# Performance work log

Measured on AMD Instinct MI355X. Metric: run time of the kernel, lower is better.

## Reference

```python
import jax, jax.numpy as jnp
import numpy as np

B = 2
DZ, DY, DX = 10, 200, 176
N_PER = 100000                      # active voxels per batch element
C_IN, C_MID, C_OUT = 64, 32, 64
STRIDE = 8

_OFFS = np.stack(np.meshgrid(np.arange(3), np.arange(3), np.arange(3), indexing='ij'), -1).reshape(27, 3)


def _build_indices():
    rng = np.random.RandomState(0)
    rows = []
    for b in range(B):
        lin = rng.choice(DZ * DY * DX, size=N_PER, replace=False)
        z, y, x = np.unravel_index(lin, (DZ, DY, DX))
        rows.append(np.stack([np.full(N_PER, b), z, y, x], 1))
    return np.concatenate(rows, 0).astype(np.int32)


def _neighbor_maps(indices):
    # spconv-style indice generation (pure integer bookkeeping, done once in numpy)
    N = indices.shape[0]
    OZ, OY, OX = (DZ - 1) // 2 + 1, (DY - 1) // 2 + 1, (DX - 1) // 2 + 1  # k3 s2 p1 output shape
    hi = np.array([OZ, OY, OX])
    hin = np.array([DZ, DY, DX])
    i3 = indices[:, 1:4].astype(np.int64)
    cand = i3[:, None, :] + 1 - _OFFS[None]          # o*stride = i + pad - k
    valid = (cand % 2 == 0).all(-1)
    o3 = cand // 2
    valid &= ((o3 >= 0) & (o3 < hi)).all(-1)
    ob = np.broadcast_to(indices[:, 0:1], (N, 27))
    flat = np.stack([ob[valid], o3[..., 0][valid], o3[..., 1][valid], o3[..., 2][valid]], 1)
    down = np.unique(flat, axis=0).astype(np.int32)  # [M,4] stride-2 conv output coords
    M = down.shape[0]
    in_grid = -np.ones((B, DZ, DY, DX), np.int32)
    in_grid[indices[:, 0], indices[:, 1], indices[:, 2], indices[:, 3]] = np.arange(N)
    dn_grid = -np.ones((B, OZ, OY, OX), np.int32)
    dn_grid[down[:, 0], down[:, 1], down[:, 2], down[:, 3]] = np.arange(M)
    # stride-2 conv: output row m, kernel k <- input at o*2 - 1 + k
    src = down[:, None, 1:4].astype(np.int64) * 2 - 1 + _OFFS[None]
    ok = ((src >= 0) & (src < hin)).all(-1)
    srcc = np.clip(src, 0, hin - 1)
    nbr_down = np.where(ok, in_grid[down[:, 0:1], srcc[..., 0], srcc[..., 1], srcc[..., 2]], -1).astype(np.int32)
    # submanifold 3x3x3 on down coords
    d3 = down[:, None, 1:4].astype(np.int64) + (_OFFS[None] - 1)
    ok2 = ((d3 >= 0) & (d3 < hi)).all(-1)
    d3c = np.clip(d3, 0, hi - 1)
    nbr_sub = np.where(ok2, dn_grid[down[:, 0:1], d3c[..., 0], d3c[..., 1], d3c[..., 2]], -1).astype(np.int32)
    # inverse conv (transposed pairs of the stride-2 conv): input row n, kernel k <- down row at (i+1-k)/2
    o3c = np.clip(o3, 0, hi - 1)
    nbr_inv = np.where(valid, dn_grid[indices[:, 0:1], o3c[..., 0], o3c[..., 1], o3c[..., 2]], -1).astype(np.int32)
    return down, nbr_down, nbr_sub, nbr_inv


def setup_inputs():
    key = jax.random.key(0)
    ks = jax.random.split(key, 12)
    indices = _build_indices()
    down_indices, nbr_down, nbr_sub, nbr_inv = _neighbor_maps(indices)
    N = indices.shape[0]
    w = lambda k, shp: jax.random.normal(k, shp, jnp.float32) * 0.05
    l2r = np.array([[0., -1., 0., 0.], [0., 0., -1., 0.], [1., 0., 0., 0.]], np.float32)  # lidar->rect
    p2 = np.array([[721.54, 0., 609.56, 44.85], [0., 721.54, 172.85, 0.216], [0., 0., 1., 0.0027]], np.float32)
    return {
        'features': jax.random.normal(ks[0], (N, C_IN), jnp.float32),
        'W_down1': w(ks[1], (27, C_IN, C_MID)),
        'W_res': w(ks[2], (27, C_IN, C_MID)),
        'W_sub2': w(ks[3], (27, C_MID, C_MID)),
        'W_2d1': w(ks[4], (9, C_MID, C_MID)),
        'W_2d2': w(ks[5], (9, C_MID, C_MID)),
        'W_sub3': w(ks[6], (27, C_MID, C_MID)),
        'W_inv4': w(ks[7], (27, C_MID, C_OUT)),
        'bn32_g': 1.0 + 0.1 * jax.random.normal(ks[8], (7, C_MID), jnp.float32),
        'bn32_b': 0.1 * jax.random.normal(ks[9], (7, C_MID), jnp.float32),
        'bn64_g': 1.0 + 0.1 * jax.random.normal(ks[10], (2, C_OUT), jnp.float32),
        'bn64_b': 0.1 * jax.random.normal(ks[11], (2, C_OUT), jnp.float32),
        'calib_l2r': jnp.asarray(np.tile(l2r, (B, 1, 1))),
        'calib_p2': jnp.asarray(np.tile(p2, (B, 1, 1))),
        'down_indices': jnp.asarray(down_indices),
        'nbr_down': jnp.asarray(nbr_down),
        'nbr_sub': jnp.asarray(nbr_sub),
        'nbr_inv': jnp.asarray(nbr_inv),
        'stride': STRIDE,
        'batch_size': B,
    }


def _bn(x, g, b, eps=1e-3):
    # BatchNorm1d training-mode forward (batch stats, biased variance, eps=1e-3)
    m = x.mean(0)
    v = x.var(0)
    return (x - m) * jax.lax.rsqrt(v + eps) * g + b


def _gconv(feats, nbr, W):
    # spconv gather -> GEMM -> accumulate; nbr[m,k] is source row or -1
    out = jnp.zeros((nbr.shape[0], W.shape[-1]), feats.dtype)
    for k in range(W.shape[0]):
        idx = nbr[:, k]
        m = (idx >= 0).astype(feats.dtype)[:, None]
        out = out + (feats[jnp.maximum(idx, 0)] * m) @ W[k]
    return out


def _index2uv(down_indices, calib_l2r, calib_p2, stride):
    vs = 0.05 * stride
    fi = down_indices.astype(jnp.float32)
    x = fi[:, 3] * vs + (0.0 + vs / 2)
    y = fi[:, 2] * vs + (-40.0 + vs / 2)
    z = fi[:, 1] * vs + (-3.0 + vs / 2)
    pts = jnp.stack([x, y, z, jnp.ones_like(x)], 1)           # [M,4] homogeneous lidar pts
    b = down_indices[:, 0]
    rect = jnp.einsum('mi,mji->mj', pts, calib_l2r[b])        # lidar_to_rect
    rh = jnp.concatenate([rect, jnp.ones_like(rect[:, :1])], 1)
    proj = jnp.einsum('mi,mji->mj', rh, calib_p2[b])          # rect_to_img
    u = jax.lax.stop_gradient(proj[:, 0] / proj[:, 2]).astype(jnp.int32)
    v = jax.lax.stop_gradient(proj[:, 1] / proj[:, 2]).astype(jnp.int32)
    u = jnp.clip(u, 0, 1400 - stride) // stride
    v = jnp.clip(v, 0, 400 - stride) // stride
    return b, u, v


def reference(features, W_down1, W_res, W_sub2, W_2d1, W_2d2, W_sub3, W_inv4,
              bn32_g, bn32_b, bn64_g, bn64_b, calib_l2r, calib_p2,
              down_indices, nbr_down, nbr_sub, nbr_inv, stride, batch_size):
    relu = jax.nn.relu
    d3 = relu(_bn(_gconv(features, nbr_down, W_down1), bn32_g[0], bn32_b[0]))   # d3_conv1 (spconv s2)
    d3 = relu(_bn(_gconv(d3, nbr_sub, W_sub2), bn32_g[1], bn32_b[1]))           # d3_conv2 (subm)
    res = relu(_bn(_gconv(features, nbr_down, W_res), bn32_g[2], bn32_b[2]))    # resnet_layer (spconv s2)
    d3 = d3 + res
    # 3D -> 2D reprojection (index2uv) and 2D submanifold conv stage
    b, u, v = _index2uv(down_indices, calib_l2r, calib_p2, stride)
    U, V = 1400 // stride, 400 // stride
    M = d3.shape[0]
    grid = -jnp.ones((batch_size, U, V), jnp.int32)
    grid = grid.at[b, u, v].max(jnp.arange(M, dtype=jnp.int32))  # deterministic dedupe of uv collisions
    du = jnp.repeat(jnp.arange(-1, 2), 3)
    dv = jnp.tile(jnp.arange(-1, 2), 3)
    uu = u[:, None] + du[None]
    vv = v[:, None] + dv[None]
    ok = (uu >= 0) & (uu < U) & (vv >= 0) & (vv < V)
    nbr2d = jnp.where(ok, grid[b[:, None], jnp.clip(uu, 0, U - 1), jnp.clip(vv, 0, V - 1)], -1)
    d2 = relu(_bn(_gconv(d3, nbr2d, W_2d1), bn32_g[3], bn32_b[3]))              # d2_conv1
    d2 = relu(_bn(_gconv(d2, nbr2d, W_2d2), bn32_g[4], bn32_b[4]))              # d2_conv2
    d3 = _bn(d3 + d2, bn32_g[5], bn32_b[5])                                     # mid_norm_fn (no relu)
    d3 = relu(_bn(_gconv(d3, nbr_sub, W_sub3), bn32_g[6], bn32_b[6]))           # d3_conv3
    out = relu(_bn(_gconv(d3, nbr_inv, W_inv4), bn64_g[0], bn64_b[0]))          # d3_conv4 (inverse conv)
    out = _bn(out + features, bn64_g[1], bn64_b[1])                             # output_norm_fn
    return out
```

## Files before the change

kernel.cpp:

```cpp
#include <hip/hip_runtime.h>

#define NBANK 64
#define ACC_STRIDE (NBANK * 128)

typedef _Float16 half8 __attribute__((ext_vector_type(8)));
typedef float    fx4   __attribute__((ext_vector_type(4)));

__global__ void init_kernel(float* __restrict__ acc, int accN, _Float16* __restrict__ zrow,
                            int* __restrict__ grid, int gridN)
{
    int i = blockIdx.x * 256 + threadIdx.x;
    if (i < accN) acc[i] = 0.f;
    if (i < 64) ((float*)zrow)[i] = 0.f;
    if (i < gridN) grid[i] = -1;
}

struct WDesc { const float* W; _Float16* H; _Float16* L; int K, CIN, COUT, base; };
struct WArgs { WDesc d[7]; int total; };

__global__ void wsplit_all_kernel(WArgs a)
{
    int t = blockIdx.x * 256 + threadIdx.x;
    if (t >= a.total) return;
    int seg = 0;
    #pragma unroll
    for (int s = 1; s < 7; ++s) if (t >= a.d[s].base) seg = s;
    const WDesc D = a.d[seg];
    int tt   = t - D.base;
    int lane = tt & 63;
    int frag = tt >> 6;
    int NT = D.COUT >> 4, NS = D.CIN >> 5;
    int ct = frag % NT;
    int s2 = (frag / NT) % NS;
    int k  = frag / (NT * NS);
    int col = ct * 16 + (lane & 15);
    int cib = s2 * 32 + ((lane >> 4) << 3);
    half8 vh, vl;
    #pragma unroll
    for (int j = 0; j < 8; ++j) {
        float w = D.W[(size_t)(k * D.CIN + cib + j) * D.COUT + col];
        _Float16 hh = (_Float16)w;
        vh[j] = hh;
        vl[j] = (_Float16)(w - (float)hh);
    }
    *(half8*)(D.H + (size_t)tt * 8) = vh;
    *(half8*)(D.L + (size_t)tt * 8) = vl;
}

__global__ void tof16_kernel(const float* __restrict__ x, _Float16* __restrict__ h, long total)
{
    long base = ((long)blockIdx.x * 256 + threadIdx.x) * 8;
    if (base >= total) return;
    fx4 v0 = *(const fx4*)(x + base);
    fx4 v1 = *(const fx4*)(x + base + 4);
    half8 hh;
    #pragma unroll
    for (int j = 0; j < 4; ++j) { hh[j] = (_Float16)v0[j]; hh[4 + j] = (_Float16)v1[j]; }
    *(half8*)(h + base) = hh;
}

template <int CIN, int COUT, int K, bool DUAL>
__global__ __launch_bounds__(256) void gconv_mfma_kernel(
    const _Float16* __restrict__ fh, const int* __restrict__ nbr,
    const _Float16* __restrict__ Bh1, const _Float16* __restrict__ Bl1,
    const _Float16* __restrict__ Bh2, const _Float16* __restrict__ Bl2,
    const _Float16* __restrict__ zrow,
    float* __restrict__ out1, float* __restrict__ out2,
    float* __restrict__ sAcc1, float* __restrict__ sAcc2, int M)
{
    constexpr int NS   = CIN / 32;
    constexpr int NT   = COUT / 16;
    constexpr int NCH  = K * NS;
    constexpr int W2   = DUAL ? 2 : 1;
    constexpr int NARR = 2 * W2;
    constexpr int SKB  = NARR * NT;
    constexpr int NLD  = SKB / 4;

    __shared__ _Float16 ldsB[2][SKB * 512];

    const int tid  = threadIdx.x;
    const int lane = tid & 63;
    const int wv   = tid >> 6;
    const int g    = lane >> 4;
    const int r    = lane & 15;
    const int mb   = blockIdx.x * 128 + wv * 32;

    const int  row0 = mb + r;
    const int  row1 = mb + 16 + r;
    const bool ok0  = row0 < M;
    const bool ok1  = row1 < M;

    fx4 acc1[2][NT];
    fx4 acc2[DUAL ? 2 : 1][DUAL ? NT : 1];
    const fx4 zf = {0.f, 0.f, 0.f, 0.f};
    #pragma unroll
    for (int rt = 0; rt < 2; ++rt)
        #pragma unroll
        for (int ct = 0; ct < NT; ++ct) acc1[rt][ct] = zf;
    if constexpr (DUAL) {
        #pragma unroll
        for (int rt = 0; rt < 2; ++rt)
            #pragma unroll
            for (int ct = 0; ct < NT; ++ct) acc2[rt][ct] = zf;
    }

    fx4   stg[NLD];
    half8 Breg[NT][2][W2];
    half8 Aa[2], Ab[2];
    int   q0, q1;

    auto idxld = [&](int c, int& o0, int& o1) {
        if (c < NCH) {
            const int k = (NS == 2) ? (c >> 1) : c;
            o0 = ok0 ? nbr[(size_t)row0 * K + k] : -1;
            o1 = ok1 ? nbr[(size_t)row1 * K + k] : -1;
        } else { o0 = -1; o1 = -1; }
    };
    auto loadA = [&](half8 (&A)[2], int i0, int i1, int c) {
        const int cb = (NS == 2) ? ((c & 1) * 32) : 0;
        const _Float16* p0 = (i0 >= 0) ? fh + (size_t)i0 * CIN : zrow;
        const _Float16* p1 = (i1 >= 0) ? fh + (size_t)i1 * CIN : zrow;
        A[0] = *(const half8*)(p0 + cb + g * 8);
        A[1] = *(const half8*)(p1 + cb + g * 8);
    };
    auto stage_ld = [&](int c) {
        #pragma unroll
        for (int i = 0; i < NLD; ++i) {
            const int o   = tid * 16 + i * 4096;
            const int arr = o / (NT * 1024);
            const int oa  = o % (NT * 1024);
            const _Float16* ap = (arr == 0) ? Bh1 : (arr == 1) ? Bl1
                                : (arr == 2) ? Bh2 : Bl2;
            stg[i] = *(const fx4*)(ap + (size_t)c * (NT * 512) + oa / 2);
        }
    };
    auto stage_wr = [&](int buf) {
        #pragma unroll
        for (int i = 0; i < NLD; ++i)
            *(fx4*)(&ldsB[buf][0] + (tid * 16 + i * 4096) / 2) = stg[i];
    };
    auto loadB = [&](int buf) {
        #pragma unroll
        for (int ct = 0; ct < NT; ++ct)
            #pragma unroll
            for (int hl = 0; hl < 2; ++hl)
                #pragma unroll
                for (int w = 0; w < W2; ++w) {
                    const int arr = w * 2 + hl;
                    Breg[ct][hl][w] = *(const half8*)(&ldsB[buf][0] + (arr * NT + ct) * 512 + lane * 8);
                }
    };
    auto compute = [&](half8 (&A)[2]) {
        #pragma unroll
        for (int ct = 0; ct < NT; ++ct)
            #pragma unroll
            for (int rt = 0; rt < 2; ++rt) {
                acc1[rt][ct] = __builtin_amdgcn_mfma_f32_16x16x32_f16(A[rt], Breg[ct][0][0], acc1[rt][ct], 0, 0, 0);
                acc1[rt][ct] = __builtin_amdgcn_mfma_f32_16x16x32_f16(A[rt], Breg[ct][1][0], acc1[rt][ct], 0, 0, 0);
                if constexpr (DUAL) {
                    acc2[rt][ct] = __builtin_amdgcn_mfma_f32_16x16x32_f16(A[rt], Breg[ct][0][1], acc2[rt][ct], 0, 0, 0);
                    acc2[rt][ct] = __builtin_amdgcn_mfma_f32_16x16x32_f16(A[rt], Breg[ct][1][1], acc2[rt][ct], 0, 0, 0);
                }
            }
    };
    auto phase = [&](int c, half8 (&Acur)[2], half8 (&Anext)[2]) {
        const bool hn = (c + 1 < NCH);
        if (hn) stage_ld(c + 1);
        loadA(Anext, q0, q1, hn ? c + 1 : c);
        idxld(c + 2, q0, q1);
        loadB(c & 1);
        compute(Acur);
        if (hn) stage_wr((c + 1) & 1);
        __syncthreads();
    };

    idxld(0, q0, q1);
    loadA(Aa, q0, q1, 0);
    idxld(1, q0, q1);
    stage_ld(0);
    stage_wr(0);
    __syncthreads();

    #pragma unroll 1
    for (int c = 0; c < NCH; c += 2) {
        phase(c, Aa, Ab);
        if (c + 1 < NCH) phase(c + 1, Ab, Aa);
    }

    #pragma unroll
    for (int rt = 0; rt < 2; ++rt)
        #pragma unroll
        for (int q = 0; q < 4; ++q) {
            const int rw = mb + rt * 16 + g * 4 + q;
            if (rw < M) {
                #pragma unroll
                for (int ct = 0; ct < NT; ++ct) {
                    out1[(size_t)rw * COUT + ct * 16 + r] = acc1[rt][ct][q];
                    if constexpr (DUAL)
                        out2[(size_t)rw * COUT + ct * 16 + r] = acc2[rt][ct][q];
                }
            }
        }

    #pragma unroll
    for (int ct = 0; ct < NT; ++ct) {
        float s1 = 0.f, p1 = 0.f, s2v = 0.f, p2v = 0.f;
        #pragma unroll
        for (int rt = 0; rt < 2; ++rt)
            #pragma unroll
            for (int q = 0; q < 4; ++q) {
                const int rw = mb + rt * 16 + g * 4 + q;
                if (rw < M) {
                    float v = acc1[rt][ct][q];
                    s1 += v; p1 += v * v;
                    if constexpr (DUAL) { float u = acc2[rt][ct][q]; s2v += u; p2v += u * u; }
                }
            }
        s1 += __shfl_xor(s1, 16, 64); s1 += __shfl_xor(s1, 32, 64);
        p1 += __shfl_xor(p1, 16, 64); p1 += __shfl_xor(p1, 32, 64);
        if constexpr (DUAL) {
            s2v += __shfl_xor(s2v, 16, 64); s2v += __shfl_xor(s2v, 32, 64);
            p2v += __shfl_xor(p2v, 16, 64); p2v += __shfl_xor(p2v, 32, 64);
        }
        if (lane < 16) {
            float* a = sAcc1 + ((blockIdx.x * 4 + wv) & (NBANK - 1)) * 128;
            atomicAdd(&a[ct * 16 + lane], s1);
            atomicAdd(&a[64 + ct * 16 + lane], p1);
            if constexpr (DUAL) {
                float* b2 = sAcc2 + ((blockIdx.x * 4 + wv) & (NBANK - 1)) * 128;
                atomicAdd(&b2[ct * 16 + lane], s2v);
                atomicAdd(&b2[64 + ct * 16 + lane], p2v);
            }
        }
    }
}

template <int C>
__global__ void finalize_kernel(const float* __restrict__ acc, const float* __restrict__ g,
                                const float* __restrict__ b, int M, float* __restrict__ sc)
{
    int c = threadIdx.x;
    if (c < C) {
        float s = 0.f, s2 = 0.f;
        #pragma unroll 8
        for (int k = 0; k < NBANK; ++k) {
            s  += acc[k * 128 + c];
            s2 += acc[k * 128 + 64 + c];
        }
        float inv  = 1.f / (float)M;
        float mean = s * inv;
        float var  = s2 * inv - mean * mean;
        float rstd = rsqrtf(var + 1e-3f);
        float scale = g[c] * rstd;
        sc[c]      = scale;
        sc[64 + c] = b[c] - mean * scale;
    }
}

template <int C>
__global__ __launch_bounds__(256) void apply_kernel(
    const float* __restrict__ x, const float* __restrict__ sc,
    const float* __restrict__ addv, float* __restrict__ outf,
    _Float16* __restrict__ outh, float* __restrict__ statAcc, long total, int relu)
{
    __shared__ float shS[64], shS2[64];
    if (statAcc && threadIdx.x < 64) { shS[threadIdx.x] = 0.f; shS2[threadIdx.x] = 0.f; }

    float s[8], s2[8];
    #pragma unroll
    for (int j = 0; j < 8; ++j) { s[j] = 0.f; s2[j] = 0.f; }

    const long start  = ((long)blockIdx.x * 256 + threadIdx.x) * 8;
    const long stride = (long)gridDim.x * 256 * 8;
    const int  c0     = (int)(start & (C - 1));
    float sA[8], sB[8];
    #pragma unroll
    for (int j = 0; j < 8; ++j) { sA[j] = sc[c0 + j]; sB[j] = sc[64 + c0 + j]; }

    for (long base = start; base < total; base += stride) {
        fx4 v0 = *(const fx4*)(x + base);
        fx4 v1 = *(const fx4*)(x + base + 4);
        float v[8] = {v0[0], v0[1], v0[2], v0[3], v1[0], v1[1], v1[2], v1[3]};
        fx4 a0 = {0.f, 0.f, 0.f, 0.f}, a1 = {0.f, 0.f, 0.f, 0.f};
        if (addv) { a0 = *(const fx4*)(addv + base); a1 = *(const fx4*)(addv + base + 4); }
        #pragma unroll
        for (int j = 0; j < 8; ++j) {
            float w = v[j] * sA[j] + sB[j];
            if (relu) w = fmaxf(w, 0.f);
            if (addv) w += (j < 4) ? a0[j] : a1[j - 4];
            v[j] = w;
            s[j] += w; s2[j] += w * w;
        }
        if (outf) {
            *(fx4*)(outf + base)     = fx4{v[0], v[1], v[2], v[3]};
            *(fx4*)(outf + base + 4) = fx4{v[4], v[5], v[6], v[7]};
        }
        if (outh) {
            half8 hh;
            #pragma unroll
            for (int j = 0; j < 8; ++j) hh[j] = (_Float16)v[j];
            *(half8*)(outh + base) = hh;
        }
    }

    if (statAcc) {
        __syncthreads();
        #pragma unroll
        for (int j = 0; j < 8; ++j) {
            atomicAdd(&shS[c0 + j], s[j]);
            atomicAdd(&shS2[c0 + j], s2[j]);
        }
        __syncthreads();
        if (threadIdx.x < C) {
            float* a = statAcc + (blockIdx.x & (NBANK - 1)) * 128;
            atomicAdd(&a[threadIdx.x], shS[threadIdx.x]);
            atomicAdd(&a[64 + threadIdx.x], shS2[threadIdx.x]);
        }
    }
}

__global__ void uv_scatter_kernel(const int* __restrict__ down, const float* __restrict__ l2r,
                                  const float* __restrict__ p2, int M,
                                  int* __restrict__ ub, int* __restrict__ vb,
                                  int* __restrict__ grid)
{
    __shared__ int shCell[256];
    const int m = blockIdx.x * 256 + threadIdx.x;
    int cell = -1;
    if (m < M) {
        int b = down[4 * m];
        float fz = (float)down[4 * m + 1];
        float fy = (float)down[4 * m + 2];
        float fx = (float)down[4 * m + 3];
        const float vs = 0.4f;
        float x = __fadd_rn(__fmul_rn(fx, vs), 0.2f);
        float y = __fadd_rn(__fmul_rn(fy, vs), -39.79999923706054688f);
        float z = __fadd_rn(__fmul_rn(fz, vs), -2.79999995231628418f);
        double xd = (double)x, yd = (double)y, zd = (double)z;
        const float* L = l2r + b * 12;
        double r0 = (double)L[0] * xd + (double)L[1] * yd + (double)L[2]  * zd + (double)L[3];
        double r1 = (double)L[4] * xd + (double)L[5] * yd + (double)L[6]  * zd + (double)L[7];
        double r2 = (double)L[8] * xd + (double)L[9] * yd + (double)L[10] * zd + (double)L[11];
        const float* P = p2 + b * 12;
        double p0 = (double)P[0] * r0 + (double)P[1] * r1 + (double)P[2]  * r2 + (double)P[3];
        double p1 = (double)P[4] * r0 + (double)P[5] * r1 + (double)P[6]  * r2 + (double)P[7];
        double pz = (double)P[8] * r0 + (double)P[9] * r1 + (double)P[10] * r2 + (double)P[11];
        int u = (int)(p0 / pz);
        int v = (int)(p1 / pz);
        u = min(max(u, 0), 1392) >> 3;
        v = min(max(v, 0), 392) >> 3;
        ub[m] = u;
        vb[m] = v;
        cell = (b * 175 + u) * 50 + v;
    }
    shCell[threadIdx.x] = cell;
    __syncthreads();
    if (m < M) {
        const bool last = (threadIdx.x == 255) || (shCell[threadIdx.x + 1] != cell);
        if (last) atomicMax(&grid[cell], m);
    }
}

__global__ void grid_copy_kernel(const int* __restrict__ grid, int* __restrict__ grid2, int n)
{
    int i = blockIdx.x * 256 + threadIdx.x;
    if (i < n) grid2[i] = grid[i];
}

__global__ void nbr2d_kernel(const int* __restrict__ down, const int* __restrict__ ub,
                             const int* __restrict__ vb, const int* __restrict__ grid,
                             int* __restrict__ nb2, int M)
{
    int m = blockIdx.x * 256 + threadIdx.x;
    if (m >= M) return;
    int b = down[4 * m];
    int u = ub[m], v = vb[m];
    #pragma unroll
    for (int j = 0; j < 9; ++j) {
        int uu = u + j / 3 - 1;
        int vv = v + j % 3 - 1;
        int val = -1;
        if (uu >= 0 && uu < 175 && vv >= 0 && vv < 50) val = grid[(b * 175 + uu) * 50 + vv];
        nb2[m * 9 + j] = val;
    }
}

extern "C" void kernel_launch(void* const* d_in, const int* in_sizes, int n_in,
                              void* d_out, int out_size, void* d_ws, size_t ws_size,
                              hipStream_t stream)
{
    const float* feats  = (const float*)d_in[0];
    const float* Wd1    = (const float*)d_in[1];
    const float* Wres   = (const float*)d_in[2];
    const float* Wsub2  = (const float*)d_in[3];
    const float* W2d1   = (const float*)d_in[4];
    const float* W2d2   = (const float*)d_in[5];
    const float* Wsub3  = (const float*)d_in[6];
    const float* Winv4  = (const float*)d_in[7];
    const float* bn32g  = (const float*)d_in[8];
    const float* bn32b  = (const float*)d_in[9];
    const float* bn64g  = (const float*)d_in[10];
    const float* bn64b  = (const float*)d_in[11];
    const float* l2r    = (const float*)d_in[12];
    const float* p2c    = (const float*)d_in[13];
    const int*   down   = (const int*)d_in[14];
    const int*   nbrD   = (const int*)d_in[15];
    const int*   nbrS   = (const int*)d_in[16];
    const int*   nbrI   = (const int*)d_in[17];

    const int N = in_sizes[0] / 64;
    const int M = in_sizes[14] / 4;

    char* ws = (char*)d_ws;
    size_t off = 0;
    auto alloc = [&](size_t bytes) -> void* {
        void* p = ws + off;
        off = (off + bytes + 255) & ~(size_t)255;
        return p;
    };
    float* t0    = (float*)alloc((size_t)M * 32 * 4);
    float* t1    = (float*)alloc((size_t)M * 32 * 4);
    float* t2    = (float*)alloc((size_t)M * 32 * 4);
    int*   ub    = (int*)alloc((size_t)M * 4);
    int*   vb    = (int*)alloc((size_t)M * 4);
    int*   nb2   = (int*)alloc((size_t)M * 9 * 4);
    int*   grid  = (int*)alloc((size_t)2 * 175 * 50 * 4);
    int*   grid2 = (int*)alloc((size_t)2 * 175 * 50 * 4);
    float* acc   = (float*)alloc((size_t)9 * ACC_STRIDE * 4);
    float* sc    = (float*)alloc((size_t)9 * 128 * 4);
    _Float16* zrow = (_Float16*)alloc(128 * 2);
    _Float16* fhh = (_Float16*)alloc((size_t)N * 64 * 2);
    _Float16* t0h = (_Float16*)alloc((size_t)M * 32 * 2);
    _Float16* t1h = (_Float16*)alloc((size_t)M * 32 * 2);
    _Float16* t2h = (_Float16*)alloc((size_t)M * 32 * 2);
    _Float16* wD1h = (_Float16*)alloc((size_t)55296 * 2);
    _Float16* wD1l = (_Float16*)alloc((size_t)55296 * 2);
    _Float16* wReh = (_Float16*)alloc((size_t)55296 * 2);
    _Float16* wRel = (_Float16*)alloc((size_t)55296 * 2);
    _Float16* wS2h = (_Float16*)alloc((size_t)27648 * 2);
    _Float16* wS2l = (_Float16*)alloc((size_t)27648 * 2);
    _Float16* w21h = (_Float16*)alloc((size_t)9216 * 2);
    _Float16* w21l = (_Float16*)alloc((size_t)9216 * 2);
    _Float16* w22h = (_Float16*)alloc((size_t)9216 * 2);
    _Float16* w22l = (_Float16*)alloc((size_t)9216 * 2);
    _Float16* wS3h = (_Float16*)alloc((size_t)27648 * 2);
    _Float16* wS3l = (_Float16*)alloc((size_t)27648 * 2);
    _Float16* wI4h = (_Float16*)alloc((size_t)55296 * 2);
    _Float16* wI4l = (_Float16*)alloc((size_t)55296 * 2);
    float* g0 = (float*)d_out;

    const int accN = 9 * ACC_STRIDE;
    init_kernel<<<(accN + 255) / 256, 256, 0, stream>>>(acc, accN, zrow, grid, 17500);

    WArgs wa;
    auto mkd = [](const float* W, _Float16* H, _Float16* L, int K, int CIN, int COUT, int base) {
        WDesc d; d.W = W; d.H = H; d.L = L; d.K = K; d.CIN = CIN; d.COUT = COUT; d.base = base;
        return d;
    };
    int b0 = 0;
    wa.d[0] = mkd(Wd1,   wD1h, wD1l, 27, 64, 32, b0); b0 += 27 * 64 * 32 / 8;
    wa.d[1] = mkd(Wres,  wReh, wRel, 27, 64, 32, b0); b0 += 27 * 64 * 32 / 8;
    wa.d[2] = mkd(Wsub2, wS2h, wS2l, 27, 32, 32, b0); b0 += 27 * 32 * 32 / 8;
    wa.d[3] = mkd(W2d1,  w21h, w21l,  9, 32, 32, b0); b0 += 9 * 32 * 32 / 8;
    wa.d[4] = mkd(W2d2,  w22h, w22l,  9, 32, 32, b0); b0 += 9 * 32 * 32 / 8;
    wa.d[5] = mkd(Wsub3, wS3h, wS3l, 27, 32, 32, b0); b0 += 27 * 32 * 32 / 8;
    wa.d[6] = mkd(Winv4, wI4h, wI4l, 27, 32, 64, b0); b0 += 27 * 32 * 64 / 8;
    wa.total = b0;
    wsplit_all_kernel<<<(wa.total + 255) / 256, 256, 0, stream>>>(wa);

    const long totF = (long)N * 64;
    tof16_kernel<<<(int)((totF / 8 + 255) / 256), 256, 0, stream>>>(feats, fhh, totF);

    const int  gT    = (M + 127) / 128;
    const int  gTN   = (N + 127) / 128;
    const long tot32 = (long)M * 32;
    const long tot64 = (long)N * 64;
    const int  ab32  = min((int)((tot32 / 8 + 255) / 256), 2560);
    const int  ab64  = min((int)((tot64 / 8 + 255) / 256), 2560);
    const int  gM    = (M + 255) / 256;

    gconv_mfma_kernel<64, 32, 27, true><<<gT, 256, 0, stream>>>(
        fhh, nbrD, wD1h, wD1l, wReh, wRel, zrow, t0, t1, acc + 0 * ACC_STRIDE, acc + 1 * ACC_STRIDE, M);
    finalize_kernel<32><<<1, 64, 0, stream>>>(acc + 0 * ACC_STRIDE, bn32g + 0 * 32, bn32b + 0 * 32, M, sc + 0 * 128);
    finalize_kernel<32><<<1, 64, 0, stream>>>(acc + 1 * ACC_STRIDE, bn32g + 2 * 32, bn32b + 2 * 32, M, sc + 1 * 128);
    apply_kernel<32><<<ab32, 256, 0, stream>>>(t0, sc + 0 * 128, nullptr, nullptr, t0h, nullptr, tot32, 1);
    apply_kernel<32><<<ab32, 256, 0, stream>>>(t1, sc + 1 * 128, nullptr, t1, nullptr, nullptr, tot32, 1);

    gconv_mfma_kernel<32, 32, 27, false><<<gT, 256, 0, stream>>>(
        t0h, nbrS, wS2h, wS2l, nullptr, nullptr, zrow, t2, nullptr, acc + 2 * ACC_STRIDE, nullptr, M);
    finalize_kernel<32><<<1, 64, 0, stream>>>(acc + 2 * ACC_STRIDE, bn32g + 1 * 32, bn32b + 1 * 32, M, sc + 2 * 128);
    apply_kernel<32><<<ab32, 256, 0, stream>>>(t2, sc + 2 * 128, t1, t2, t2h, nullptr, tot32, 1);

    uv_scatter_kernel<<<gM, 256, 0, stream>>>(down, l2r, p2c, M, ub, vb, grid);
    grid_copy_kernel<<<(17500 + 255) / 256, 256, 0, stream>>>(grid, grid2, 17500);
    nbr2d_kernel<<<gM, 256, 0, stream>>>(down, ub, vb, grid2, nb2, M);

    gconv_mfma_kernel<32, 32, 9, false><<<gT, 256, 0, stream>>>(
        t2h, nb2, w21h, w21l, nullptr, nullptr, zrow, t0, nullptr, acc + 3 * ACC_STRIDE, nullptr, M);
    finalize_kernel<32><<<1, 64, 0, stream>>>(acc + 3 * ACC_STRIDE, bn32g + 3 * 32, bn32b + 3 * 32, M, sc + 3 * 128);
    apply_kernel<32><<<ab32, 256, 0, stream>>>(t0, sc + 3 * 128, nullptr, nullptr, t0h, nullptr, tot32, 1);

    gconv_mfma_kernel<32, 32, 9, false><<<gT, 256, 0, stream>>>(
        t0h, nb2, w22h, w22l, nullptr, nullptr, zrow, t1, nullptr, acc + 4 * ACC_STRIDE, nullptr, M);
    finalize_kernel<32><<<1, 64, 0, stream>>>(acc + 4 * ACC_STRIDE, bn32g + 4 * 32, bn32b + 4 * 32, M, sc + 4 * 128);
    apply_kernel<32><<<ab32, 256, 0, stream>>>(t1, sc + 4 * 128, t2, t1, nullptr, acc + 5 * ACC_STRIDE, tot32, 1);
    finalize_kernel<32><<<1, 64, 0, stream>>>(acc + 5 * ACC_STRIDE, bn32g + 5 * 32, bn32b + 5 * 32, M, sc + 5 * 128);
    apply_kernel<32><<<ab32, 256, 0, stream>>>(t1, sc + 5 * 128, nullptr, nullptr, t1h, nullptr, tot32, 0);

    gconv_mfma_kernel<32, 32, 27, false><<<gT, 256, 0, stream>>>(
        t1h, nbrS, wS3h, wS3l, nullptr, nullptr, zrow, t0, nullptr, acc + 6 * ACC_STRIDE, nullptr, M);
    finalize_kernel<32><<<1, 64, 0, stream>>>(acc + 6 * ACC_STRIDE, bn32g + 6 * 32, bn32b + 6 * 32, M, sc + 6 * 128);
    apply_kernel<32><<<ab32, 256, 0, stream>>>(t0, sc + 6 * 128, nullptr, nullptr, t0h, nullptr, tot32, 1);

    gconv_mfma_kernel<32, 64, 27, false><<<gTN, 256, 0, stream>>>(
        t0h, nbrI, wI4h, wI4l, nullptr, nullptr, zrow, g0, nullptr, acc + 7 * ACC_STRIDE, nullptr, N);
    finalize_kernel<64><<<1, 64, 0, stream>>>(acc + 7 * ACC_STRIDE, bn64g + 0 * 64, bn64b + 0 * 64, N, sc + 7 * 128);
    apply_kernel<64><<<ab64, 256, 0, stream>>>(g0, sc + 7 * 128, feats, g0, nullptr, acc + 8 * ACC_STRIDE, tot64, 1);
    finalize_kernel<64><<<1, 64, 0, stream>>>(acc + 8 * ACC_STRIDE, bn64g + 1 * 64, bn64b + 1 * 64, N, sc + 8 * 128);
    apply_kernel<64><<<ab64, 256, 0, stream>>>(g0, sc + 8 * 128, nullptr, (float*)d_out, nullptr, nullptr, tot64, 0);
}
```

Baseline: 567.0 us.

## Process two K-chunks per barrier in gather-conv MFMA pipeline

Restructures the gather-convolution main loop so each pipeline stage stages, gathers and computes two consecutive K-chunks, with ping-pong A registers and a double-size LDS weight buffer. This halves the number of __syncthreads barriers and gives more independent gathers in flight per stage, plus s_setprio around the MFMA section. The trade-off is doubled LDS and staging/A-fragment registers, which may reduce occupancy, plus a tail path for an odd chunk count.

```diff
diff --git a/kernel.cpp b/kernel.cpp
--- a/kernel.cpp
+++ b/kernel.cpp
@@ -68,15 +68,17 @@
     float* __restrict__ out1, float* __restrict__ out2,
     float* __restrict__ sAcc1, float* __restrict__ sAcc2, int M)
 {
-    constexpr int NS   = CIN / 32;
-    constexpr int NT   = COUT / 16;
-    constexpr int NCH  = K * NS;
-    constexpr int W2   = DUAL ? 2 : 1;
-    constexpr int NARR = 2 * W2;
-    constexpr int SKB  = NARR * NT;
-    constexpr int NLD  = SKB / 4;
-
-    __shared__ _Float16 ldsB[2][SKB * 512];
+    constexpr int NS    = CIN / 32;
+    constexpr int NT    = COUT / 16;
+    constexpr int NCH   = K * NS;
+    constexpr int NPAIR = NCH / 2;
+    constexpr int W2    = DUAL ? 2 : 1;
+    constexpr int NARR  = 2 * W2;
+    constexpr int SKB   = NARR * NT;
+    constexpr int NLD   = SKB / 4;
+    constexpr int CHH   = SKB * 512;
+
+    __shared__ _Float16 ldsB[2][2 * CHH];
 
     const int tid  = threadIdx.x;
     const int lane = tid & 63;
@@ -104,17 +106,17 @@
             for (int ct = 0; ct < NT; ++ct) acc2[rt][ct] = zf;
     }
 
-    fx4   stg[NLD];
+    fx4   stg[2][NLD];
     half8 Breg[NT][2][W2];
-    half8 Aa[2], Ab[2];
-    int   q0, q1;
-
-    auto idxld = [&](int c, int& o0, int& o1) {
+    half8 Aa0[2], Aa1[2], Ab0[2], Ab1[2];
+    int   e0, e1, o0, o1;
+
+    auto idxld = [&](int c, int& i0, int& i1) {
         if (c < NCH) {
             const int k = (NS == 2) ? (c >> 1) : c;
-            o0 = ok0 ? nbr[(size_t)row0 * K + k] : -1;
-            o1 = ok1 ? nbr[(size_t)row1 * K + k] : -1;
-        } else { o0 = -1; o1 = -1; }
+            i0 = ok0 ? nbr[(size_t)row0 * K + k] : -1;
+            i1 = ok1 ? nbr[(size_t)row1 * K + k] : -1;
+        } else { i0 = -1; i1 = -1; }
     };
     auto loadA = [&](half8 (&A)[2], int i0, int i1, int c) {
         const int cb = (NS == 2) ? ((c & 1) * 32) : 0;
@@ -123,23 +125,29 @@
         A[0] = *(const half8*)(p0 + cb + g * 8);
         A[1] = *(const half8*)(p1 + cb + g * 8);
     };
-    auto stage_ld = [&](int c) {
-        #pragma unroll
-        for (int i = 0; i < NLD; ++i) {
-            const int o   = tid * 16 + i * 4096;
-            const int arr = o / (NT * 1024);
-            const int oa  = o % (NT * 1024);
-            const _Float16* ap = (arr == 0) ? Bh1 : (arr == 1) ? Bl1
-                                : (arr == 2) ? Bh2 : Bl2;
-            stg[i] = *(const fx4*)(ap + (size_t)c * (NT * 512) + oa / 2);
-        }
-    };
-    auto stage_wr = [&](int buf) {
-        #pragma unroll
-        for (int i = 0; i < NLD; ++i)
-            *(fx4*)(&ldsB[buf][0] + (tid * 16 + i * 4096) / 2) = stg[i];
-    };
-    auto loadB = [&](int buf) {
+    auto stage_ld2 = [&](int c) {
+        #pragma unroll
+        for (int sub = 0; sub < 2; ++sub) {
+            const int cc = (c + sub < NCH) ? (c + sub) : (NCH - 1);
+            #pragma unroll
+            for (int i = 0; i < NLD; ++i) {
+                const int o   = tid * 16 + i * 4096;
+                const int arr = o / (NT * 1024);
+                const int oa  = o % (NT * 1024);
+                const _Float16* ap = (arr == 0) ? Bh1 : (arr == 1) ? Bl1
+                                    : (arr == 2) ? Bh2 : Bl2;
+                stg[sub][i] = *(const fx4*)(ap + (size_t)cc * (NT * 512) + oa / 2);
+            }
+        }
+    };
+    auto stage_wr2 = [&](int buf) {
+        #pragma unroll
+        for (int sub = 0; sub < 2; ++sub)
+            #pragma unroll
+            for (int i = 0; i < NLD; ++i)
+                *(fx4*)(&ldsB[buf][sub * CHH] + (tid * 16 + i * 4096) / 2) = stg[sub][i];
+    };
+    auto loadB = [&](int buf, int sub) {
         #pragma unroll
         for (int ct = 0; ct < NT; ++ct)
             #pragma unroll
@@ -147,7 +155,7 @@
                 #pragma unroll
                 for (int w = 0; w < W2; ++w) {
                     const int arr = w * 2 + hl;
-                    Breg[ct][hl][w] = *(const half8*)(&ldsB[buf][0] + (arr * NT + ct) * 512 + lane * 8);
+                    Breg[ct][hl][w] = *(const half8*)(&ldsB[buf][sub * CHH] + (arr * NT + ct) * 512 + lane * 8);
                 }
     };
     auto compute = [&](half8 (&A)[2]) {
@@ -163,28 +171,54 @@
                 }
             }
     };
-    auto phase = [&](int c, half8 (&Acur)[2], half8 (&Anext)[2]) {
-        const bool hn = (c + 1 < NCH);
-        if (hn) stage_ld(c + 1);
-        loadA(Anext, q0, q1, hn ? c + 1 : c);
-        idxld(c + 2, q0, q1);
-        loadB(c & 1);
-        compute(Acur);
-        if (hn) stage_wr((c + 1) & 1);
-        __syncthreads();
-    };
-
-    idxld(0, q0, q1);
-    loadA(Aa, q0, q1, 0);
-    idxld(1, q0, q1);
-    stage_ld(0);
-    stage_wr(0);
+
+    idxld(0, e0, e1); idxld(1, o0, o1);
+    loadA(Aa0, e0, e1, 0); loadA(Aa1, o0, o1, 1);
+    idxld(2, e0, e1); idxld(3, o0, o1);
+    stage_ld2(0);
+    stage_wr2(0);
     __syncthreads();
 
-    #pragma unroll 1
-    for (int c = 0; c < NCH; c += 2) {
-        phase(c, Aa, Ab);
-        if (c + 1 < NCH) phase(c + 1, Ab, Aa);
+    int c = 0;
+    while (true) {
+        {
+            const int  buf = (c >> 1) & 1;
+            const bool hn  = (c + 2 < NCH);
+            if (hn) stage_ld2(c + 2);
+            loadA(Ab0, e0, e1, c + 2);
+            loadA(Ab1, o0, o1, c + 3);
+            idxld(c + 4, e0, e1); idxld(c + 5, o0, o1);
+            __builtin_amdgcn_s_setprio(1);
+            loadB(buf, 0); compute(Aa0);
+            loadB(buf, 1); compute(Aa1);
+            __builtin_amdgcn_s_setprio(0);
+            if (hn) stage_wr2(buf ^ 1);
+            __syncthreads();
+        }
+        c += 2;
+        if (c + 1 >= NCH) break;
+        {
+            const int  buf = (c >> 1) & 1;
+            const bool hn  = (c + 2 < NCH);
+            if (hn) stage_ld2(c + 2);
+            loadA(Aa0, e0, e1, c + 2);
+            loadA(Aa1, o0, o1, c + 3);
+            idxld(c + 4, e0, e1); idxld(c + 5, o0, o1);
+            __builtin_amdgcn_s_setprio(1);
+            loadB(buf, 0); compute(Ab0);
+            loadB(buf, 1); compute(Ab1);
+            __builtin_amdgcn_s_setprio(0);
+            if (hn) stage_wr2(buf ^ 1);
+            __syncthreads();
+        }
+        c += 2;
+        if (c + 1 >= NCH) break;
+    }
+    if constexpr (NCH & 1) {
+        const int buf = ((NCH - 1) >> 1) & 1;
+        loadB(buf, 0);
+        if constexpr (NPAIR & 1) compute(Ab0);
+        else                     compute(Aa0);
     }
 
     #pragma unroll
```

After: 572.4 us. About the same (+1.0%).

## Deepen gather pipeline to triple-buffered A rows with setprio and manual barriers

Applied to the files above, without the earlier changes.

Reworks the gconv MFMA main loop from double- to triple-buffered A operand registers, so neighbour rows are gathered two chunks ahead and indices three ahead. This hides more of the random gather latency behind compute. It also raises wave priority around the LDS B loads and MFMA block, and replaces __syncthreads with an explicit lgkmcnt wait, s_barrier and sched_barrier. The loop is unrolled by six with a static tail, which raises register pressure and could lower occupancy.

```diff
diff --git a/kernel.cpp b/kernel.cpp
--- a/kernel.cpp
+++ b/kernel.cpp
@@ -75,6 +75,7 @@
     constexpr int NARR = 2 * W2;
     constexpr int SKB  = NARR * NT;
     constexpr int NLD  = SKB / 4;
+    static_assert(NCH % 6 == 0 || NCH % 6 == 3, "tail handling assumes NCH%6 in {0,3}");
 
     __shared__ _Float16 ldsB[2][SKB * 512];
 
@@ -106,15 +107,15 @@
 
     fx4   stg[NLD];
     half8 Breg[NT][2][W2];
-    half8 Aa[2], Ab[2];
-    int   q0, q1;
-
-    auto idxld = [&](int c, int& o0, int& o1) {
+    half8 A0[2], A1[2], A2[2];
+    int qa0, qa1, qb0, qb1, qc0, qc1;
+
+    auto idxld = [&](int c, int& i0, int& i1) {
         if (c < NCH) {
             const int k = (NS == 2) ? (c >> 1) : c;
-            o0 = ok0 ? nbr[(size_t)row0 * K + k] : -1;
-            o1 = ok1 ? nbr[(size_t)row1 * K + k] : -1;
-        } else { o0 = -1; o1 = -1; }
+            i0 = ok0 ? nbr[(size_t)row0 * K + k] : -1;
+            i1 = ok1 ? nbr[(size_t)row1 * K + k] : -1;
+        } else { i0 = -1; i1 = -1; }
     };
     auto loadA = [&](half8 (&A)[2], int i0, int i1, int c) {
         const int cb = (NS == 2) ? ((c & 1) * 32) : 0;
@@ -163,28 +164,46 @@
                 }
             }
     };
-    auto phase = [&](int c, half8 (&Acur)[2], half8 (&Anext)[2]) {
+    auto phase = [&](half8 (&Acur)[2], half8 (&Aload)[2], int i0, int i1,
+                     int& f0, int& f1, int c, int rb, int wb) {
         const bool hn = (c + 1 < NCH);
         if (hn) stage_ld(c + 1);
-        loadA(Anext, q0, q1, hn ? c + 1 : c);
-        idxld(c + 2, q0, q1);
-        loadB(c & 1);
+        loadA(Aload, i0, i1, c + 2);
+        idxld(c + 3, f0, f1);
+        __builtin_amdgcn_s_setprio(1);
+        loadB(rb);
         compute(Acur);
-        if (hn) stage_wr((c + 1) & 1);
-        __syncthreads();
-    };
-
-    idxld(0, q0, q1);
-    loadA(Aa, q0, q1, 0);
-    idxld(1, q0, q1);
+        __builtin_amdgcn_s_setprio(0);
+        if (hn) stage_wr(wb);
+        asm volatile("s_waitcnt lgkmcnt(0)" ::: "memory");
+        __builtin_amdgcn_s_barrier();
+        __builtin_amdgcn_sched_barrier(0);
+    };
+
+    idxld(0, qa0, qa1);
+    loadA(A0, qa0, qa1, 0);
+    idxld(1, qb0, qb1);
+    loadA(A1, qb0, qb1, 1);
+    idxld(2, qc0, qc1);
     stage_ld(0);
     stage_wr(0);
-    __syncthreads();
-
-    #pragma unroll 1
-    for (int c = 0; c < NCH; c += 2) {
-        phase(c, Aa, Ab);
-        if (c + 1 < NCH) phase(c + 1, Ab, Aa);
+    asm volatile("s_waitcnt lgkmcnt(0)" ::: "memory");
+    __builtin_amdgcn_s_barrier();
+    __builtin_amdgcn_sched_barrier(0);
+
+    int c = 0;
+    for (; c + 6 <= NCH; c += 6) {
+        phase(A0, A2, qc0, qc1, qa0, qa1, c + 0, 0, 1);
+        phase(A1, A0, qa0, qa1, qb0, qb1, c + 1, 1, 0);
+        phase(A2, A1, qb0, qb1, qc0, qc1, c + 2, 0, 1);
+        phase(A0, A2, qc0, qc1, qa0, qa1, c + 3, 1, 0);
+        phase(A1, A0, qa0, qa1, qb0, qb1, c + 4, 0, 1);
+        phase(A2, A1, qb0, qb1, qc0, qc1, c + 5, 1, 0);
+    }
+    if constexpr (NCH % 6 == 3) {
+        phase(A0, A2, qc0, qc1, qa0, qa1, c + 0, 0, 1);
+        phase(A1, A0, qa0, qa1, qb0, qb1, c + 1, 1, 0);
+        phase(A2, A1, qb0, qb1, qc0, qc1, c + 2, 0, 1);
     }
 
     #pragma unroll
```

After: 563.4 us. About the same (-0.6%).
